# Kernel tuning notes

Measured on AMD Instinct MI355X. Metric: run time of the kernel, lower is better.

The kernel has to match this reference:

```python
import jax, jax.numpy as jnp
import numpy as np

B, T, C = 4, 2048, 1024
HQ, HKV = 16, 4          # n_query_head, n_kv_head
D = C // HQ              # head_dim = 64
G = HQ // HKV            # group_size = 4


def setup_inputs() -> dict:
    key = jax.random.key(0)
    ks = jax.random.split(key, 9)
    s = 0.02
    return {
        "x":  jax.random.normal(ks[0], (B, T, C), dtype=jnp.float32),
        "Wq": jax.random.normal(ks[1], (C, C), dtype=jnp.float32) * s,
        "bq": jnp.zeros((C,), dtype=jnp.float32),
        "Wk": jax.random.normal(ks[2], (C, HKV * D), dtype=jnp.float32) * s,
        "bk": jnp.zeros((HKV * D,), dtype=jnp.float32),
        "Wv": jax.random.normal(ks[3], (C, HKV * D), dtype=jnp.float32) * s,
        "bv": jnp.zeros((HKV * D,), dtype=jnp.float32),
        "Wo": jax.random.normal(ks[4], (C, C), dtype=jnp.float32) * s,
        "bo": jnp.zeros((C,), dtype=jnp.float32),
    }


def reference(x, Wq, bq, Wk, bk, Wv, bv, Wo, bo):
    b, t, c = x.shape
    # projections
    q = x @ Wq + bq                                   # [B,T,C]
    k = x @ Wk + bk                                   # [B,T,HKV*D]
    v = x @ Wv + bv
    # b t (h d) -> b h t d ; then split query heads (h g): head = h*G + g
    q = q.reshape(b, t, HQ, D).transpose(0, 2, 1, 3)            # [B,HQ,T,D]
    q = q.reshape(b, HKV, G, t, D)                              # [B,h,g,T,D]
    k = k.reshape(b, t, HKV, D).transpose(0, 2, 1, 3)           # [B,h,T,D]
    v = v.reshape(b, t, HKV, D).transpose(0, 2, 1, 3)           # [B,h,T,D]

    scale = jnp.sqrt(jnp.float32(D))
    att = jnp.einsum('bhgqd,bhkd->bhgqk', q, k) / scale         # [B,h,g,T,T]
    causal = jnp.tril(jnp.ones((t, t), dtype=bool))             # [T,T]
    att = jnp.where(causal, att, -jnp.inf)
    att = jax.nn.softmax(att, axis=-1)

    y = jnp.einsum('bhgqk,bhkd->bhgqd', att, v)                 # [B,h,g,T,D]
    # b h g q d -> b q (h g) d -> b q C
    y = y.transpose(0, 3, 1, 2, 4).reshape(b, t, c)
    y = y @ Wo + bo
    # original returns att_weights as 'b g h q k'
    att_weights = att.transpose(0, 2, 1, 3, 4)
    return y, att_weights
```

## Files before the change

### kernel.cpp

```cpp
#include <hip/hip_runtime.h>
#include <hip/hip_bf16.h>

#define Bb 4
#define Tt 2048
#define Ccc 1024
#define HQn 16
#define HKVn 4
#define Dd 64
#define Gg 4

typedef unsigned short u16;
typedef short bf16x8 __attribute__((ext_vector_type(8)));
typedef float f32x4 __attribute__((ext_vector_type(4)));
static_assert(sizeof(bf16x8) == 16, "bf16x8 must be 16B");

static __device__ __forceinline__ u16 f2b(float f) {
  union { __hip_bfloat16 b; u16 u; } cv;
  cv.b = __float2bfloat16(f);
  return cv.u;
}

__global__ void cvt_bf16(const float* __restrict__ in, u16* __restrict__ out, int n4) {
  int i = blockIdx.x * blockDim.x + threadIdx.x;
  if (i < n4) {
    float4 v = ((const float4*)in)[i];
    ushort4 o;
    o.x = f2b(v.x); o.y = f2b(v.y); o.z = f2b(v.z); o.w = f2b(v.w);
    ((ushort4*)out)[i] = o;
  }
}

__global__ void tpose(const float* __restrict__ in, u16* __restrict__ out, int R, int C) {
  __shared__ float tile[32][33];
  int c0 = blockIdx.x * 32, r0 = blockIdx.y * 32;
  int tx = threadIdx.x, ty = threadIdx.y;
  for (int i = ty; i < 32; i += 8)
    tile[i][tx] = in[(size_t)(r0 + i) * C + c0 + tx];
  __syncthreads();
  for (int i = ty; i < 32; i += 8)
    out[(size_t)(c0 + i) * R + r0 + tx] = f2b(tile[tx][i]);
}

__global__ void vtrans(const u16* __restrict__ v, u16* __restrict__ vt) {
  __shared__ u16 tile[32][33];
  int bh = blockIdx.z;
  int b = bh >> 2, h = bh & 3;
  int t0 = blockIdx.x * 32;
  int d0 = blockIdx.y * 32;
  int tx = threadIdx.x, ty = threadIdx.y;
  for (int i = ty; i < 32; i += 8)
    tile[i][tx] = v[(size_t)(b * Tt + t0 + i) * (HKVn * Dd) + h * Dd + d0 + tx];
  __syncthreads();
  for (int i = ty; i < 32; i += 8)
    vt[(size_t)(bh * Dd + d0 + i) * Tt + t0 + tx] = tile[tx][i];
}

template <int OUT_BF16>
__global__ __launch_bounds__(256) void gemm_bf16(
    const u16* __restrict__ A, const u16* __restrict__ BT,
    const float* __restrict__ bias, void* __restrict__ out,
    int M, int N, int K, float scale) {
  __shared__ __align__(16) u16 As[128][40];
  __shared__ __align__(16) u16 Bs[128][40];
  const int tid = threadIdx.x;
  const int wave = tid >> 6, lane = tid & 63, l15 = lane & 15, quad = lane >> 4;
  const int m0 = blockIdx.y * 128, n0 = blockIdx.x * 128;
  const int wm = (wave >> 1) * 64, wn = (wave & 1) * 64;
  const int arow = tid >> 1, acol = (tid & 1) * 16;
  f32x4 acc[4][4] = {};
  for (int k0 = 0; k0 < K; k0 += 32) {
    bf16x8 av0 = *(const bf16x8*)(A + (size_t)(m0 + arow) * K + k0 + acol);
    bf16x8 av1 = *(const bf16x8*)(A + (size_t)(m0 + arow) * K + k0 + acol + 8);
    bf16x8 bv0 = *(const bf16x8*)(BT + (size_t)(n0 + arow) * K + k0 + acol);
    bf16x8 bv1 = *(const bf16x8*)(BT + (size_t)(n0 + arow) * K + k0 + acol + 8);
    *(bf16x8*)&As[arow][acol + 0] = av0;
    *(bf16x8*)&As[arow][acol + 8] = av1;
    *(bf16x8*)&Bs[arow][acol + 0] = bv0;
    *(bf16x8*)&Bs[arow][acol + 8] = bv1;
    __syncthreads();
    bf16x8 af[4], bfr[4];
#pragma unroll
    for (int i = 0; i < 4; ++i) af[i] = *(const bf16x8*)&As[wm + i * 16 + l15][quad * 8];
#pragma unroll
    for (int i = 0; i < 4; ++i) bfr[i] = *(const bf16x8*)&Bs[wn + i * 16 + l15][quad * 8];
#pragma unroll
    for (int i = 0; i < 4; ++i)
#pragma unroll
      for (int j = 0; j < 4; ++j)
        acc[i][j] = __builtin_amdgcn_mfma_f32_16x16x32_bf16(af[i], bfr[j], acc[i][j], 0, 0, 0);
    __syncthreads();
  }
#pragma unroll
  for (int i = 0; i < 4; ++i) {
    const int row = m0 + wm + i * 16 + quad * 4;
#pragma unroll
    for (int j = 0; j < 4; ++j) {
      const int col = n0 + wn + j * 16 + l15;
      const float bval = bias[col];
#pragma unroll
      for (int r = 0; r < 4; ++r) {
        float v = (acc[i][j][r] + bval) * scale;
        if (OUT_BF16)
          ((u16*)out)[(size_t)(row + r) * N + col] = f2b(v);
        else
          ((float*)out)[(size_t)(row + r) * N + col] = v;
      }
    }
  }
}

__global__ __launch_bounds__(256) void attn(
    const u16* __restrict__ Q,
    const u16* __restrict__ K,
    const u16* __restrict__ Vt,
    float* __restrict__ att,
    u16* __restrict__ Y) {
  __shared__ __align__(16) u16 Qs[128][72];
  __shared__ __align__(16) u16 Ks[64][72];
  __shared__ __align__(16) u16 Vs[64][72];
  __shared__ __align__(16) u16 Ps[128][72];

  const int bid = blockIdx.x;
  const int qt = bid & 15, g = (bid >> 4) & 3, h = (bid >> 6) & 3, b = bid >> 8;
  const int head = h * Gg + g;
  const int q0 = qt * 128;
  const int tid = threadIdx.x;
  const int wave = tid >> 6, lane = tid & 63, l15 = lane & 15, quad = lane >> 4;
  const int w32 = wave * 32;
  const int nkt = (q0 + 128) >> 6;

  {
    const int row = tid >> 1, half = (tid & 1) * 32;
    const u16* src = Q + (size_t)(b * Tt + q0 + row) * Ccc + head * Dd + half;
    bf16x8 v0 = *(const bf16x8*)(src);
    bf16x8 v1 = *(const bf16x8*)(src + 8);
    bf16x8 v2 = *(const bf16x8*)(src + 16);
    bf16x8 v3 = *(const bf16x8*)(src + 24);
    *(bf16x8*)&Qs[row][half + 0]  = v0;
    *(bf16x8*)&Qs[row][half + 8]  = v1;
    *(bf16x8*)&Qs[row][half + 16] = v2;
    *(bf16x8*)&Qs[row][half + 24] = v3;
  }
  __syncthreads();

  float m_run[2][4], l_run[2][4];
#pragma unroll
  for (int ms = 0; ms < 2; ++ms)
#pragma unroll
    for (int r = 0; r < 4; ++r) { m_run[ms][r] = -1e30f; l_run[ms][r] = 0.f; }

  const int kkrow = tid >> 2, kpart = (tid & 3) * 16;

  for (int kt = 0; kt < nkt; ++kt) {
    const int k0 = kt * 64;
    {
      const u16* src = K + (size_t)(b * Tt + k0 + kkrow) * (HKVn * Dd) + h * Dd + kpart;
      bf16x8 v0 = *(const bf16x8*)(src);
      bf16x8 v1 = *(const bf16x8*)(src + 8);
      *(bf16x8*)&Ks[kkrow][kpart + 0] = v0;
      *(bf16x8*)&Ks[kkrow][kpart + 8] = v1;
    }
    __syncthreads();
    f32x4 s[2][4] = {};
#pragma unroll
    for (int c = 0; c < 2; ++c) {
      bf16x8 aq[2], bk[4];
#pragma unroll
      for (int ms = 0; ms < 2; ++ms)
        aq[ms] = *(const bf16x8*)&Qs[w32 + ms * 16 + l15][c * 32 + quad * 8];
#pragma unroll
      for (int ns = 0; ns < 4; ++ns)
        bk[ns] = *(const bf16x8*)&Ks[ns * 16 + l15][c * 32 + quad * 8];
#pragma unroll
      for (int ms = 0; ms < 2; ++ms)
#pragma unroll
        for (int ns = 0; ns < 4; ++ns)
          s[ms][ns] = __builtin_amdgcn_mfma_f32_16x16x32_bf16(aq[ms], bk[ns], s[ms][ns], 0, 0, 0);
    }
#pragma unroll
    for (int ms = 0; ms < 2; ++ms) {
#pragma unroll
      for (int r = 0; r < 4; ++r) {
        const int qg = q0 + w32 + ms * 16 + quad * 4 + r;
#pragma unroll
        for (int ns = 0; ns < 4; ++ns)
          if (k0 + ns * 16 + l15 > qg) s[ms][ns][r] = -1e30f;
        float tm = fmaxf(fmaxf(s[ms][0][r], s[ms][1][r]), fmaxf(s[ms][2][r], s[ms][3][r]));
#pragma unroll
        for (int off = 1; off < 16; off <<= 1)
          tm = fmaxf(tm, __shfl_xor(tm, off, 16));
        const float mnew = fmaxf(m_run[ms][r], tm);
        float ls = __expf(s[ms][0][r] - mnew) + __expf(s[ms][1][r] - mnew)
                 + __expf(s[ms][2][r] - mnew) + __expf(s[ms][3][r] - mnew);
#pragma unroll
        for (int off = 1; off < 16; off <<= 1)
          ls += __shfl_xor(ls, off, 16);
        l_run[ms][r] = l_run[ms][r] * __expf(m_run[ms][r] - mnew) + ls;
        m_run[ms][r] = mnew;
      }
    }
    __syncthreads();
  }

  float rl[2][4];
#pragma unroll
  for (int ms = 0; ms < 2; ++ms)
#pragma unroll
    for (int r = 0; r < 4; ++r) rl[ms][r] = 1.f / l_run[ms][r];

  f32x4 o[2][4] = {};
  const size_t att_base = ((size_t)((b * Gg + g) * HKVn + h)) * Tt * Tt;

  for (int kt = 0; kt < nkt; ++kt) {
    const int k0 = kt * 64;
    {
      const u16* src = K + (size_t)(b * Tt + k0 + kkrow) * (HKVn * Dd) + h * Dd + kpart;
      bf16x8 v0 = *(const bf16x8*)(src);
      bf16x8 v1 = *(const bf16x8*)(src + 8);
      const u16* vsrc = Vt + (size_t)((b * HKVn + h) * Dd + kkrow) * Tt + k0 + kpart;
      bf16x8 w0 = *(const bf16x8*)(vsrc);
      bf16x8 w1 = *(const bf16x8*)(vsrc + 8);
      *(bf16x8*)&Ks[kkrow][kpart + 0] = v0;
      *(bf16x8*)&Ks[kkrow][kpart + 8] = v1;
      *(bf16x8*)&Vs[kkrow][kpart + 0] = w0;
      *(bf16x8*)&Vs[kkrow][kpart + 8] = w1;
    }
    __syncthreads();
    f32x4 s[2][4] = {};
#pragma unroll
    for (int c = 0; c < 2; ++c) {
      bf16x8 aq[2], bk[4];
#pragma unroll
      for (int ms = 0; ms < 2; ++ms)
        aq[ms] = *(const bf16x8*)&Qs[w32 + ms * 16 + l15][c * 32 + quad * 8];
#pragma unroll
      for (int ns = 0; ns < 4; ++ns)
        bk[ns] = *(const bf16x8*)&Ks[ns * 16 + l15][c * 32 + quad * 8];
#pragma unroll
      for (int ms = 0; ms < 2; ++ms)
#pragma unroll
        for (int ns = 0; ns < 4; ++ns)
          s[ms][ns] = __builtin_amdgcn_mfma_f32_16x16x32_bf16(aq[ms], bk[ns], s[ms][ns], 0, 0, 0);
    }
#pragma unroll
    for (int ms = 0; ms < 2; ++ms) {
#pragma unroll
      for (int r = 0; r < 4; ++r) {
        const int qg = q0 + w32 + ms * 16 + quad * 4 + r;
#pragma unroll
        for (int ns = 0; ns < 4; ++ns) {
          const int kg = k0 + ns * 16 + l15;
          float p = (kg > qg) ? 0.f : __expf(s[ms][ns][r] - m_run[ms][r]) * rl[ms][r];
          att[att_base + (size_t)qg * Tt + kg] = p;
          Ps[w32 + ms * 16 + quad * 4 + r][ns * 16 + l15] = f2b(p);
        }
      }
    }
#pragma unroll
    for (int c = 0; c < 2; ++c) {
      bf16x8 ap[2], bv2[4];
#pragma unroll
      for (int ms = 0; ms < 2; ++ms)
        ap[ms] = *(const bf16x8*)&Ps[w32 + ms * 16 + l15][c * 32 + quad * 8];
#pragma unroll
      for (int nd = 0; nd < 4; ++nd)
        bv2[nd] = *(const bf16x8*)&Vs[nd * 16 + l15][c * 32 + quad * 8];
#pragma unroll
      for (int ms = 0; ms < 2; ++ms)
#pragma unroll
        for (int nd = 0; nd < 4; ++nd)
          o[ms][nd] = __builtin_amdgcn_mfma_f32_16x16x32_bf16(ap[ms], bv2[nd], o[ms][nd], 0, 0, 0);
    }
    __syncthreads();
  }

  const int zstart = nkt * 64;
  if (zstart < Tt) {
    const int zw4 = (Tt - zstart) >> 2;
    const float4 z4 = make_float4(0.f, 0.f, 0.f, 0.f);
    for (int rr = 0; rr < 128; ++rr) {
      float4* rowp = (float4*)(att + att_base + (size_t)(q0 + rr) * Tt + zstart);
      for (int cc = tid; cc < zw4; cc += 256) rowp[cc] = z4;
    }
  }

#pragma unroll
  for (int ms = 0; ms < 2; ++ms)
#pragma unroll
    for (int nd = 0; nd < 4; ++nd)
#pragma unroll
      for (int r = 0; r < 4; ++r) {
        const int qg = q0 + w32 + ms * 16 + quad * 4 + r;
        Y[(size_t)(b * Tt + qg) * Ccc + head * Dd + nd * 16 + l15] = f2b(o[ms][nd][r]);
      }
}

extern "C" void kernel_launch(void* const* d_in, const int* in_sizes, int n_in,
                              void* d_out, int out_size, void* d_ws, size_t ws_size,
                              hipStream_t stream) {
  const float* x  = (const float*)d_in[0];
  const float* Wq = (const float*)d_in[1];
  const float* bq = (const float*)d_in[2];
  const float* Wk = (const float*)d_in[3];
  const float* bk = (const float*)d_in[4];
  const float* Wv = (const float*)d_in[5];
  const float* bv = (const float*)d_in[6];
  const float* Wo = (const float*)d_in[7];
  const float* bo = (const float*)d_in[8];
  float* out = (float*)d_out;

  char* ws = (char*)d_ws;
  u16* xb   = (u16*)(ws + 0);
  u16* WqT  = (u16*)(ws + 16777216);
  u16* WkT  = (u16*)(ws + 18874368);
  u16* WvT  = (u16*)(ws + 19398656);
  u16* WoT  = (u16*)(ws + 19922944);
  u16* Qb   = (u16*)(ws + 22020096);
  u16* Kb   = (u16*)(ws + 38797312);
  u16* Vb   = (u16*)(ws + 42991616);
  u16* Vtb  = (u16*)(ws + 47185920);
  u16* Yatt = (u16*)(ws + 51380224);

  cvt_bf16<<<8192, 256, 0, stream>>>(x, xb, 8388608 / 4);
  tpose<<<dim3(32, 32), dim3(32, 8), 0, stream>>>(Wq, WqT, 1024, 1024);
  tpose<<<dim3(8, 32),  dim3(32, 8), 0, stream>>>(Wk, WkT, 1024, 256);
  tpose<<<dim3(8, 32),  dim3(32, 8), 0, stream>>>(Wv, WvT, 1024, 256);
  tpose<<<dim3(32, 32), dim3(32, 8), 0, stream>>>(Wo, WoT, 1024, 1024);

  gemm_bf16<1><<<dim3(8, 64), 256, 0, stream>>>(xb, WqT, bq, Qb, 8192, 1024, 1024, 0.125f);
  gemm_bf16<1><<<dim3(2, 64), 256, 0, stream>>>(xb, WkT, bk, Kb, 8192, 256, 1024, 1.0f);
  gemm_bf16<1><<<dim3(2, 64), 256, 0, stream>>>(xb, WvT, bv, Vb, 8192, 256, 1024, 1.0f);

  vtrans<<<dim3(64, 2, 16), dim3(32, 8), 0, stream>>>(Vb, Vtb);

  attn<<<1024, 256, 0, stream>>>(Qb, Kb, Vtb, out + 8388608, Yatt);

  gemm_bf16<0><<<dim3(8, 64), 256, 0, stream>>>(Yatt, WoT, bo, out, 8192, 1024, 1024, 1.0f);
}
```

Measured before the change: 1.433 ms.

## Split attention into single-pass flash kernel plus separate probability-writing kernel

The two-pass attention kernel, which computed row statistics and then recomputed scores to write probabilities and accumulate PV, becomes a single-pass online-softmax flash kernel. That kernel saves per-row max and reciprocal sum to a workspace buffer. A second kernel, launched over 128x128 tiles, recomputes QK^T, writes the normalized probabilities with vectorized stores, and zero-fills the upper-triangle tiles in parallel. The aim is to spread the large attention-weight write across many blocks and take it out of the serialized per-query-tile loop. The cost is an extra QK^T recompute and reuse of the xb workspace region for the stats, which is safe only because xb is no longer needed at that point.

```diff
diff --git a/kernel.cpp b/kernel.cpp
--- a/kernel.cpp
+++ b/kernel.cpp
@@ -109,11 +109,12 @@
   }
 }
 
-__global__ __launch_bounds__(256) void attn(
+__global__ __launch_bounds__(256) void attn_flash(
     const u16* __restrict__ Q,
     const u16* __restrict__ K,
     const u16* __restrict__ Vt,
-    float* __restrict__ att,
+    float* __restrict__ mOut,
+    float* __restrict__ rlOut,
     u16* __restrict__ Y) {
   __shared__ __align__(16) u16 Qs[128][72];
   __shared__ __align__(16) u16 Ks[64][72];
@@ -148,68 +149,9 @@
   for (int ms = 0; ms < 2; ++ms)
 #pragma unroll
     for (int r = 0; r < 4; ++r) { m_run[ms][r] = -1e30f; l_run[ms][r] = 0.f; }
+  f32x4 o[2][4] = {};
 
   const int kkrow = tid >> 2, kpart = (tid & 3) * 16;
-
-  for (int kt = 0; kt < nkt; ++kt) {
-    const int k0 = kt * 64;
-    {
-      const u16* src = K + (size_t)(b * Tt + k0 + kkrow) * (HKVn * Dd) + h * Dd + kpart;
-      bf16x8 v0 = *(const bf16x8*)(src);
-      bf16x8 v1 = *(const bf16x8*)(src + 8);
-      *(bf16x8*)&Ks[kkrow][kpart + 0] = v0;
-      *(bf16x8*)&Ks[kkrow][kpart + 8] = v1;
-    }
-    __syncthreads();
-    f32x4 s[2][4] = {};
-#pragma unroll
-    for (int c = 0; c < 2; ++c) {
-      bf16x8 aq[2], bk[4];
-#pragma unroll
-      for (int ms = 0; ms < 2; ++ms)
-        aq[ms] = *(const bf16x8*)&Qs[w32 + ms * 16 + l15][c * 32 + quad * 8];
-#pragma unroll
-      for (int ns = 0; ns < 4; ++ns)
-        bk[ns] = *(const bf16x8*)&Ks[ns * 16 + l15][c * 32 + quad * 8];
-#pragma unroll
-      for (int ms = 0; ms < 2; ++ms)
-#pragma unroll
-        for (int ns = 0; ns < 4; ++ns)
-          s[ms][ns] = __builtin_amdgcn_mfma_f32_16x16x32_bf16(aq[ms], bk[ns], s[ms][ns], 0, 0, 0);
-    }
-#pragma unroll
-    for (int ms = 0; ms < 2; ++ms) {
-#pragma unroll
-      for (int r = 0; r < 4; ++r) {
-        const int qg = q0 + w32 + ms * 16 + quad * 4 + r;
-#pragma unroll
-        for (int ns = 0; ns < 4; ++ns)
-          if (k0 + ns * 16 + l15 > qg) s[ms][ns][r] = -1e30f;
-        float tm = fmaxf(fmaxf(s[ms][0][r], s[ms][1][r]), fmaxf(s[ms][2][r], s[ms][3][r]));
-#pragma unroll
-        for (int off = 1; off < 16; off <<= 1)
-          tm = fmaxf(tm, __shfl_xor(tm, off, 16));
-        const float mnew = fmaxf(m_run[ms][r], tm);
-        float ls = __expf(s[ms][0][r] - mnew) + __expf(s[ms][1][r] - mnew)
-                 + __expf(s[ms][2][r] - mnew) + __expf(s[ms][3][r] - mnew);
-#pragma unroll
-        for (int off = 1; off < 16; off <<= 1)
-          ls += __shfl_xor(ls, off, 16);
-        l_run[ms][r] = l_run[ms][r] * __expf(m_run[ms][r] - mnew) + ls;
-        m_run[ms][r] = mnew;
-      }
-    }
-    __syncthreads();
-  }
-
-  float rl[2][4];
-#pragma unroll
-  for (int ms = 0; ms < 2; ++ms)
-#pragma unroll
-    for (int r = 0; r < 4; ++r) rl[ms][r] = 1.f / l_run[ms][r];
-
-  f32x4 o[2][4] = {};
-  const size_t att_base = ((size_t)((b * Gg + g) * HKVn + h)) * Tt * Tt;
 
   for (int kt = 0; kt < nkt; ++kt) {
     const int k0 = kt * 64;
@@ -226,6 +168,7 @@
       *(bf16x8*)&Vs[kkrow][kpart + 8] = w1;
     }
     __syncthreads();
+
     f32x4 s[2][4] = {};
 #pragma unroll
     for (int c = 0; c < 2; ++c) {
@@ -242,20 +185,39 @@
         for (int ns = 0; ns < 4; ++ns)
           s[ms][ns] = __builtin_amdgcn_mfma_f32_16x16x32_bf16(aq[ms], bk[ns], s[ms][ns], 0, 0, 0);
     }
+
 #pragma unroll
     for (int ms = 0; ms < 2; ++ms) {
 #pragma unroll
       for (int r = 0; r < 4; ++r) {
         const int qg = q0 + w32 + ms * 16 + quad * 4 + r;
 #pragma unroll
+        for (int ns = 0; ns < 4; ++ns)
+          if (k0 + ns * 16 + l15 > qg) s[ms][ns][r] = -1e30f;
+        float tm = fmaxf(fmaxf(s[ms][0][r], s[ms][1][r]), fmaxf(s[ms][2][r], s[ms][3][r]));
+#pragma unroll
+        for (int off = 1; off < 16; off <<= 1)
+          tm = fmaxf(tm, __shfl_xor(tm, off, 16));
+        const float mnew = fmaxf(m_run[ms][r], tm);
+        const float corr = __expf(m_run[ms][r] - mnew);
+        const int prow = w32 + ms * 16 + quad * 4 + r;
+        float ls = 0.f;
+#pragma unroll
         for (int ns = 0; ns < 4; ++ns) {
-          const int kg = k0 + ns * 16 + l15;
-          float p = (kg > qg) ? 0.f : __expf(s[ms][ns][r] - m_run[ms][r]) * rl[ms][r];
-          att[att_base + (size_t)qg * Tt + kg] = p;
-          Ps[w32 + ms * 16 + quad * 4 + r][ns * 16 + l15] = f2b(p);
+          float p = __expf(s[ms][ns][r] - mnew);
+          Ps[prow][ns * 16 + l15] = f2b(p);
+          ls += p;
         }
+#pragma unroll
+        for (int off = 1; off < 16; off <<= 1)
+          ls += __shfl_xor(ls, off, 16);
+        l_run[ms][r] = l_run[ms][r] * corr + ls;
+        m_run[ms][r] = mnew;
+#pragma unroll
+        for (int nd = 0; nd < 4; ++nd) o[ms][nd][r] *= corr;
       }
     }
+
 #pragma unroll
     for (int c = 0; c < 2; ++c) {
       bf16x8 ap[2], bv2[4];
@@ -274,15 +236,11 @@
     __syncthreads();
   }
 
-  const int zstart = nkt * 64;
-  if (zstart < Tt) {
-    const int zw4 = (Tt - zstart) >> 2;
-    const float4 z4 = make_float4(0.f, 0.f, 0.f, 0.f);
-    for (int rr = 0; rr < 128; ++rr) {
-      float4* rowp = (float4*)(att + att_base + (size_t)(q0 + rr) * Tt + zstart);
-      for (int cc = tid; cc < zw4; cc += 256) rowp[cc] = z4;
-    }
-  }
+  float rl[2][4];
+#pragma unroll
+  for (int ms = 0; ms < 2; ++ms)
+#pragma unroll
+    for (int r = 0; r < 4; ++r) rl[ms][r] = 1.f / l_run[ms][r];
 
 #pragma unroll
   for (int ms = 0; ms < 2; ++ms)
@@ -291,8 +249,112 @@
 #pragma unroll
       for (int r = 0; r < 4; ++r) {
         const int qg = q0 + w32 + ms * 16 + quad * 4 + r;
-        Y[(size_t)(b * Tt + qg) * Ccc + head * Dd + nd * 16 + l15] = f2b(o[ms][nd][r]);
+        Y[(size_t)(b * Tt + qg) * Ccc + head * Dd + nd * 16 + l15] = f2b(o[ms][nd][r] * rl[ms][r]);
       }
+
+  if (l15 == 0) {
+    const int mbase = (b * HQn + head) * Tt;
+#pragma unroll
+    for (int ms = 0; ms < 2; ++ms)
+#pragma unroll
+      for (int r = 0; r < 4; ++r) {
+        const int qg = q0 + w32 + ms * 16 + quad * 4 + r;
+        mOut[mbase + qg]  = m_run[ms][r];
+        rlOut[mbase + qg] = rl[ms][r];
+      }
+  }
+}
+
+__global__ __launch_bounds__(256) void att_write(
+    const u16* __restrict__ Q,
+    const u16* __restrict__ K,
+    const float* __restrict__ mBuf,
+    const float* __restrict__ rlBuf,
+    float* __restrict__ att) {
+  const int bid = blockIdx.x;
+  const int mat = bid >> 8, rem = bid & 255;
+  const int qt = rem >> 4, kt = rem & 15;
+  const int q0 = qt * 128, k0 = kt * 128;
+  const size_t att_base = (size_t)mat * (size_t)Tt * (size_t)Tt;
+  const int tid = threadIdx.x;
+
+  if (kt > qt) {
+    const int rr = tid >> 5, c4 = tid & 31;
+    f32x4* base = (f32x4*)(att + att_base);
+    const f32x4 z = {0.f, 0.f, 0.f, 0.f};
+#pragma unroll 4
+    for (int i = rr; i < 128; i += 8)
+      base[(((size_t)(q0 + i) * Tt + k0) >> 2) + c4] = z;
+    return;
+  }
+
+  __shared__ __align__(16) u16 Qs[128][72];
+  __shared__ __align__(16) u16 Ks[128][72];
+  const int b = mat >> 4, g = (mat >> 2) & 3, h = mat & 3;
+  const int head = h * Gg + g;
+  const int wave = tid >> 6, lane = tid & 63, l15 = lane & 15, quad = lane >> 4;
+
+  {
+    const int row = tid >> 1, half = (tid & 1) * 32;
+    const u16* qsrc = Q + (size_t)(b * Tt + q0 + row) * Ccc + head * Dd + half;
+    bf16x8 a0 = *(const bf16x8*)(qsrc);
+    bf16x8 a1 = *(const bf16x8*)(qsrc + 8);
+    bf16x8 a2 = *(const bf16x8*)(qsrc + 16);
+    bf16x8 a3 = *(const bf16x8*)(qsrc + 24);
+    const u16* ksrc = K + (size_t)(b * Tt + k0 + row) * (HKVn * Dd) + h * Dd + half;
+    bf16x8 c0 = *(const bf16x8*)(ksrc);
+    bf16x8 c1 = *(const bf16x8*)(ksrc + 8);
+    bf16x8 c2 = *(const bf16x8*)(ksrc + 16);
+    bf16x8 c3 = *(const bf16x8*)(ksrc + 24);
+    *(bf16x8*)&Qs[row][half + 0]  = a0;
+    *(bf16x8*)&Qs[row][half + 8]  = a1;
+    *(bf16x8*)&Qs[row][half + 16] = a2;
+    *(bf16x8*)&Qs[row][half + 24] = a3;
+    *(bf16x8*)&Ks[row][half + 0]  = c0;
+    *(bf16x8*)&Ks[row][half + 8]  = c1;
+    *(bf16x8*)&Ks[row][half + 16] = c2;
+    *(bf16x8*)&Ks[row][half + 24] = c3;
+  }
+  __syncthreads();
+
+  const int wq = wave * 32;
+  f32x4 acc[8][2] = {};
+#pragma unroll
+  for (int c = 0; c < 2; ++c) {
+    bf16x8 kf[8], qf[2];
+#pragma unroll
+    for (int ns = 0; ns < 8; ++ns)
+      kf[ns] = *(const bf16x8*)&Ks[ns * 16 + l15][c * 32 + quad * 8];
+#pragma unroll
+    for (int ms = 0; ms < 2; ++ms)
+      qf[ms] = *(const bf16x8*)&Qs[wq + ms * 16 + l15][c * 32 + quad * 8];
+#pragma unroll
+    for (int ns = 0; ns < 8; ++ns)
+#pragma unroll
+      for (int ms = 0; ms < 2; ++ms)
+        acc[ns][ms] = __builtin_amdgcn_mfma_f32_16x16x32_bf16(kf[ns], qf[ms], acc[ns][ms], 0, 0, 0);
+  }
+
+  const int mbase = (b * HQn + head) * Tt;
+  const bool diag = (kt == qt);
+#pragma unroll
+  for (int ms = 0; ms < 2; ++ms) {
+    const int q = q0 + wq + ms * 16 + l15;
+    const float mq = mBuf[mbase + q];
+    const float rq = rlBuf[mbase + q];
+#pragma unroll
+    for (int ns = 0; ns < 8; ++ns) {
+      const int kk = k0 + ns * 16 + quad * 4;
+      f32x4 pv;
+#pragma unroll
+      for (int r = 0; r < 4; ++r) {
+        float p = __expf(acc[ns][ms][r] - mq) * rq;
+        if (diag && (kk + r > q)) p = 0.f;
+        pv[r] = p;
+      }
+      *(f32x4*)(att + att_base + (size_t)q * Tt + kk) = pv;
+    }
+  }
 }
 
 extern "C" void kernel_launch(void* const* d_in, const int* in_sizes, int n_in,
@@ -320,6 +382,8 @@
   u16* Vb   = (u16*)(ws + 42991616);
   u16* Vtb  = (u16*)(ws + 47185920);
   u16* Yatt = (u16*)(ws + 51380224);
+  float* mBuf  = (float*)(ws + 0);
+  float* rlBuf = (float*)(ws + 524288);
 
   cvt_bf16<<<8192, 256, 0, stream>>>(x, xb, 8388608 / 4);
   tpose<<<dim3(32, 32), dim3(32, 8), 0, stream>>>(Wq, WqT, 1024, 1024);
@@ -333,7 +397,8 @@
 
   vtrans<<<dim3(64, 2, 16), dim3(32, 8), 0, stream>>>(Vb, Vtb);
 
-  attn<<<1024, 256, 0, stream>>>(Qb, Kb, Vtb, out + 8388608, Yatt);
+  attn_flash<<<1024, 256, 0, stream>>>(Qb, Kb, Vtb, mBuf, rlBuf, Yatt);
+  att_write<<<16384, 256, 0, stream>>>(Qb, Kb, mBuf, rlBuf, out + 8388608);
 
   gemm_bf16<0><<<dim3(8, 64), 256, 0, stream>>>(Yatt, WoT, bo, out, 8192, 1024, 1024, 1.0f);
 }
```

New measurement: 1.505 ms. +5.0%, slower.
